# Kernel tuning notes

Hardware: AMD Instinct MI355X
Metric: run time of the kernel (lower is better)

The kernel has to match this reference:

```python
import jax, jax.numpy as jnp
import numpy as np

K = 64
M = 256
V = 5000

def setup_inputs() -> dict:
    key = jax.random.key(0)
    ks = jax.random.split(key, 8)
    feat_x = jax.random.normal(ks[0], (1, V, M), dtype=jnp.float32)
    feat_y = jax.random.normal(ks[1], (1, V, M), dtype=jnp.float32)
    evals_x = jnp.sort(jax.random.uniform(ks[2], (1, K), dtype=jnp.float32))
    evals_y = jnp.sort(jax.random.uniform(ks[3], (1, K), dtype=jnp.float32))
    evecs_trans_x = jax.random.normal(ks[4], (1, K, V), dtype=jnp.float32) / np.sqrt(V)
    evecs_trans_y = jax.random.normal(ks[5], (1, K, V), dtype=jnp.float32) / np.sqrt(V)
    eye = jnp.eye(K, dtype=jnp.float32)
    sqrtMk_x = (eye + 0.05 * jax.random.normal(ks[6], (K, K), dtype=jnp.float32))[None]
    sqrtMk_y = (eye + 0.05 * jax.random.normal(ks[7], (K, K), dtype=jnp.float32))[None]
    return {"feat_x": feat_x, "feat_y": feat_y, "evals_x": evals_x, "evals_y": evals_y,
            "evecs_trans_x": evecs_trans_x, "evecs_trans_y": evecs_trans_y,
            "sqrtMk_x": sqrtMk_x, "sqrtMk_y": sqrtMk_y}

LMBDA = 0.001

def _fmap(fx, fy, ex, ey, tx, ty, sx, sy):
    # squeeze batch dim of 1 (as in torch .squeeze())
    fx, fy = fx[0], fy[0]            # [V, m]
    ex, ey = ex[0], ey[0]            # [k]
    tx, ty = tx[0], ty[0]            # [k, V]
    sx, sy = sx[0], sy[0]            # [k, k]
    A = tx @ fx                      # [k, m] spectral coeffs of feat_x
    B = sy @ (ty @ fy)               # adapt_feature=True: premultiply by sqrtMk_y
    k, m = A.shape
    vec_B = B.T.reshape(m * k, 1)
    At_Ik = jnp.kron(A.T, sy)        # [m*k, k*k] (adapt_feature -> Ik = sqrtMk_y)
    first = At_Ik.T @ At_Ik          # [k^2, k^2]
    # adapt_mask=True branch
    inv_sx = jnp.linalg.inv(sx)
    lx = jnp.diag(ex)
    ly = jnp.diag(ey)
    lx_Ik = jnp.kron(lx @ inv_sx, sy)
    Ik_ly = jnp.kron(inv_sx, sy @ ly)
    Delta = lx_Ik - Ik_ly
    second = Delta.T @ Delta
    rhs = At_Ik.T @ vec_B
    op = first + LMBDA * second
    C = jnp.linalg.solve(op, rhs)
    return C.reshape(k, k).T[None]   # [1, k, k]

def reference(feat_x, feat_y, evals_x, evals_y, evecs_trans_x, evecs_trans_y, sqrtMk_x, sqrtMk_y):
    # bidirectional=False -> only Cxy (Cyx is None in the torch module)
    return _fmap(feat_x, feat_y, evals_x, evals_y, evecs_trans_x, evecs_trans_y, sqrtMk_x, sqrtMk_y)
```

## Files before the change

kernel.cpp:

```cpp
#include <hip/hip_runtime.h>

#define LMBDA 0.001f
#define NS_SY 4
#define NS_G  5
#define NS_SX 5
#define OUTER 3
#define LDP 68

#define WS_A    0
#define WS_FY   16384
#define WS_G1   32768
#define WS_T1   36864
#define WS_R2   40960
#define WS_R4   45056
#define WS_GINV 49152
#define WS_C    53248
#define WS_FYAT 57344
#define WS_FLAGS 61440

#define FMA4(ar, xs, b) { ar[0]=fmaf((xs),(b).x,ar[0]); ar[1]=fmaf((xs),(b).y,ar[1]); \
                          ar[2]=fmaf((xs),(b).z,ar[2]); ar[3]=fmaf((xs),(b).w,ar[3]); }

template<int SA, int SB>
__device__ __forceinline__ void mm64(const float* __restrict__ A,
                                     const float* __restrict__ B,
                                     int ti, int tj, float a[4][4]) {
    #pragma unroll 4
    for (int k = 0; k < 64; k += 4) {
        float4 av0 = *(const float4*)&A[(4 * ti + 0) * SA + k];
        float4 av1 = *(const float4*)&A[(4 * ti + 1) * SA + k];
        float4 av2 = *(const float4*)&A[(4 * ti + 2) * SA + k];
        float4 av3 = *(const float4*)&A[(4 * ti + 3) * SA + k];
        float4 b0 = *(const float4*)&B[(k + 0) * SB + 4 * tj];
        float4 b1 = *(const float4*)&B[(k + 1) * SB + 4 * tj];
        float4 b2 = *(const float4*)&B[(k + 2) * SB + 4 * tj];
        float4 b3 = *(const float4*)&B[(k + 3) * SB + 4 * tj];
        FMA4(a[0], av0.x, b0); FMA4(a[0], av0.y, b1); FMA4(a[0], av0.z, b2); FMA4(a[0], av0.w, b3);
        FMA4(a[1], av1.x, b0); FMA4(a[1], av1.y, b1); FMA4(a[1], av1.z, b2); FMA4(a[1], av1.w, b3);
        FMA4(a[2], av2.x, b0); FMA4(a[2], av2.y, b1); FMA4(a[2], av2.z, b2); FMA4(a[2], av2.w, b3);
        FMA4(a[3], av3.x, b0); FMA4(a[3], av3.y, b1); FMA4(a[3], av3.z, b2); FMA4(a[3], av3.w, b3);
    }
}

__device__ __forceinline__ void ns_invert(float* sM, float* sX, float* sY,
                                          int iters, int ti, int tj,
                                          int tid, float alpha)
{
    for (int idx = tid; idx < 4096; idx += 256) {
        int i = idx >> 6, j = idx & 63;
        sX[i * LDP + j] = (i == j) ? alpha : 0.f;
    }
    __syncthreads();
    for (int it = 0; it < iters; ++it) {
        float y[4][4];
        #pragma unroll
        for (int r = 0; r < 4; ++r)
            #pragma unroll
            for (int c = 0; c < 4; ++c) y[r][c] = 0.f;
        mm64<LDP, LDP>(sM, sX, ti, tj, y);
        #pragma unroll
        for (int r = 0; r < 4; ++r) {
            float4 v = {y[r][0], y[r][1], y[r][2], y[r][3]};
            *(float4*)&sY[(4 * ti + r) * 64 + 4 * tj] = v;
        }
        __syncthreads();
        float z[4][4];
        #pragma unroll
        for (int r = 0; r < 4; ++r)
            #pragma unroll
            for (int c = 0; c < 4; ++c) z[r][c] = 0.f;
        mm64<LDP, 64>(sX, sY, ti, tj, z);
        __syncthreads();
        #pragma unroll
        for (int r = 0; r < 4; ++r) {
            float4 xv = *(const float4*)&sX[(4 * ti + r) * LDP + 4 * tj];
            xv.x = 2.f * xv.x - z[r][0];
            xv.y = 2.f * xv.y - z[r][1];
            xv.z = 2.f * xv.z - z[r][2];
            xv.w = 2.f * xv.w - z[r][3];
            *(float4*)&sX[(4 * ti + r) * LDP + 4 * tj] = xv;
        }
        __syncthreads();
    }
}

__device__ __forceinline__ void wait_ge(int* flag, int target, int tid) {
    if (tid == 0) {
        while (__hip_atomic_load(flag, __ATOMIC_ACQUIRE, __HIP_MEMORY_SCOPE_AGENT) < target)
            __builtin_amdgcn_s_sleep(2);
    }
    __syncthreads();
    __threadfence();
}

__device__ __forceinline__ void signal_one(int* flag, int tid) {
    __syncthreads();
    __threadfence();
    if (tid == 0)
        (void)__hip_atomic_fetch_add(flag, 1, __ATOMIC_RELEASE, __HIP_MEMORY_SCOPE_AGENT);
}

__global__ __launch_bounds__(256, 1) void fused_fmnet(
    const float* __restrict__ fx, const float* __restrict__ fy,
    const float* __restrict__ ex, const float* __restrict__ ey,
    const float* __restrict__ tx, const float* __restrict__ ty,
    const float* __restrict__ sx, const float* __restrict__ sy,
    float* __restrict__ ws, float* __restrict__ out)
{
    extern __shared__ __align__(16) float lds[];
    int* flags = (int*)(ws + WS_FLAGS);
    const int tid = threadIdx.x;
    const int ti = tid >> 4, tj = tid & 15;
    const int bid = blockIdx.x;

    if (bid < 216) {
        float* sT = lds;
        float* sF = lds + 4352;
        const int gx = bid & 7, gy = bid >> 3;
        const int mat = gx >> 2;
        const int m0 = (gx & 3) << 6;
        const float* __restrict__ T = mat ? ty : tx;
        const float* __restrict__ F = mat ? fy : fx;
        float* __restrict__ Out = ws + (mat ? WS_FY : WS_A);

        float acc[4][4];
        #pragma unroll
        for (int r = 0; r < 4; ++r)
            #pragma unroll
            for (int c = 0; c < 4; ++c) acc[r][c] = 0.f;

        for (int sc = gy; sc * 64 < 5000; sc += 27) {
            const int v0 = sc << 6;
            int vlen = 5000 - v0; if (vlen > 64) vlen = 64;
            #pragma unroll
            for (int w = 0; w < 4; ++w) {
                const int fidx = tid + (w << 8);
                const int row = fidx >> 4, q = fidx & 15;
                const int vv = q << 2;
                if (vv < vlen) {
                    float4 val = *(const float4*)(T + (size_t)row * 5000 + v0 + vv);
                    sT[(vv + 0) * LDP + row] = val.x;
                    sT[(vv + 1) * LDP + row] = val.y;
                    sT[(vv + 2) * LDP + row] = val.z;
                    sT[(vv + 3) * LDP + row] = val.w;
                }
                if (row < vlen) {
                    *(float4*)&sF[row * LDP + (q << 2)] =
                        *(const float4*)(F + (size_t)(v0 + row) * 256 + m0 + (q << 2));
                }
            }
            __syncthreads();
            for (int v = 0; v < vlen; ++v) {
                float4 av = *(const float4*)&sT[v * LDP + 4 * ti];
                float4 bv = *(const float4*)&sF[v * LDP + 4 * tj];
                FMA4(acc[0], av.x, bv); FMA4(acc[1], av.y, bv);
                FMA4(acc[2], av.z, bv); FMA4(acc[3], av.w, bv);
            }
            __syncthreads();
        }
        #pragma unroll
        for (int r = 0; r < 4; ++r)
            #pragma unroll
            for (int c = 0; c < 4; ++c)
                atomicAdd(&Out[(4 * ti + r) * 256 + m0 + 4 * tj + c], acc[r][c]);
        __syncthreads();
        __threadfence();
        if (tid == 0) {
            (void)__hip_atomic_fetch_add(&flags[gx], 1, __ATOMIC_RELEASE, __HIP_MEMORY_SCOPE_AGENT);
            (void)__hip_atomic_fetch_add(&flags[10], 1, __ATOMIC_RELEASE, __HIP_MEMORY_SCOPE_AGENT);
        }
    } else if (bid < 220) {
        const int ch = bid - 216;
        wait_ge(&flags[ch], 27, tid);
        float* sA = lds;
        for (int idx = tid; idx < 1024; idx += 256) {
            int i = idx >> 4, m4 = (idx & 15) << 2;
            *(float4*)&sA[i * LDP + m4] =
                *(const float4*)&ws[WS_A + i * 256 + (ch << 6) + m4];
        }
        __syncthreads();
        float a[4][4];
        #pragma unroll
        for (int r = 0; r < 4; ++r)
            #pragma unroll
            for (int c = 0; c < 4; ++c) a[r][c] = 0.f;
        for (int m = 0; m < 64; m += 4) {
            float4 av[4], bv[4];
            #pragma unroll
            for (int r = 0; r < 4; ++r) av[r] = *(const float4*)&sA[(4 * ti + r) * LDP + m];
            #pragma unroll
            for (int c = 0; c < 4; ++c) bv[c] = *(const float4*)&sA[(4 * tj + c) * LDP + m];
            #pragma unroll
            for (int r = 0; r < 4; ++r)
                #pragma unroll
                for (int c = 0; c < 4; ++c)
                    a[r][c] += av[r].x * bv[c].x + av[r].y * bv[c].y
                             + av[r].z * bv[c].z + av[r].w * bv[c].w;
        }
        #pragma unroll
        for (int r = 0; r < 4; ++r)
            #pragma unroll
            for (int c = 0; c < 4; ++c)
                atomicAdd(&ws[WS_G1 + (4 * ti + r) * 64 + 4 * tj + c], a[r][c]);
        __syncthreads();
        __threadfence();
        if (tid == 0)
            (void)__hip_atomic_fetch_add(&flags[8], 1, __ATOMIC_RELEASE, __HIP_MEMORY_SCOPE_AGENT);
    } else if (bid == 220) {
        float* sSy = lds;
        float* sXx = lds + 4352;
        float* sYy = lds + 8704;
        float* sH  = lds + 12800;
        float* sV  = lds + 16896;
        for (int idx = tid; idx < 1024; idx += 256) {
            int i = idx >> 4, j4 = (idx & 15) << 2;
            *(float4*)&sSy[i * LDP + j4] = *(const float4*)&sy[i * 64 + j4];
        }
        if (tid < 64) sV[tid] = ey[tid];
        __syncthreads();
        {
            float h[4][4];
            #pragma unroll
            for (int r = 0; r < 4; ++r)
                #pragma unroll
                for (int c = 0; c < 4; ++c) h[r][c] = 0.f;
            for (int k = 0; k < 64; ++k) {
                float4 av = *(const float4*)&sSy[k * LDP + 4 * ti];
                float4 bv = *(const float4*)&sSy[k * LDP + 4 * tj];
                FMA4(h[0], av.x, bv); FMA4(h[1], av.y, bv);
                FMA4(h[2], av.z, bv); FMA4(h[3], av.w, bv);
            }
            #pragma unroll
            for (int r = 0; r < 4; ++r) {
                float4 v = {h[r][0], h[r][1], h[r][2], h[r][3]};
                *(float4*)&sH[(4 * ti + r) * 64 + 4 * tj] = v;
            }
        }
        __syncthreads();
        ns_invert(sSy, sXx, sYy, NS_SY, ti, tj, tid, 1.0f);
        {
            float h[4][4];
            #pragma unroll
            for (int r = 0; r < 4; ++r)
                #pragma unroll
                for (int c = 0; c < 4; ++c) h[r][c] = 0.f;
            for (int m = 0; m < 64; m += 4) {
                float4 av[4], bv[4];
                #pragma unroll
                for (int r = 0; r < 4; ++r) av[r] = *(const float4*)&sXx[(4 * ti + r) * LDP + m];
                #pragma unroll
                for (int c = 0; c < 4; ++c) bv[c] = *(const float4*)&sXx[(4 * tj + c) * LDP + m];
                #pragma unroll
                for (int r = 0; r < 4; ++r)
                    #pragma unroll
                    for (int c = 0; c < 4; ++c)
                        h[r][c] += av[r].x * bv[c].x + av[r].y * bv[c].y
                                 + av[r].z * bv[c].z + av[r].w * bv[c].w;
            }
            __syncthreads();
            #pragma unroll
            for (int r = 0; r < 4; ++r) {
                float4 v = {h[r][0], h[r][1], h[r][2], h[r][3]};
                *(float4*)&sSy[(4 * ti + r) * LDP + 4 * tj] = v;
            }
        }
        __syncthreads();
        {
            float a[4][4];
            #pragma unroll
            for (int r = 0; r < 4; ++r)
                #pragma unroll
                for (int c = 0; c < 4; ++c) a[r][c] = 0.f;
            #pragma unroll 4
            for (int k = 0; k < 64; k += 4) {
                float4 av[4];
                #pragma unroll
                for (int r = 0; r < 4; ++r) av[r] = *(const float4*)&sSy[(4 * ti + r) * LDP + k];
                #pragma unroll
                for (int q = 0; q < 4; ++q) {
                    float e = sV[k + q];
                    float4 bv = *(const float4*)&sH[(k + q) * 64 + 4 * tj];
                    bv.x *= e; bv.y *= e; bv.z *= e; bv.w *= e;
                    float xq[4] = {av[0].x, av[1].x, av[2].x, av[3].x};
                    if (q == 1) { xq[0]=av[0].y; xq[1]=av[1].y; xq[2]=av[2].y; xq[3]=av[3].y; }
                    if (q == 2) { xq[0]=av[0].z; xq[1]=av[1].z; xq[2]=av[2].z; xq[3]=av[3].z; }
                    if (q == 3) { xq[0]=av[0].w; xq[1]=av[1].w; xq[2]=av[2].w; xq[3]=av[3].w; }
                    #pragma unroll
                    for (int r = 0; r < 4; ++r) FMA4(a[r], xq[r], bv);
                }
            }
            #pragma unroll
            for (int r = 0; r < 4; ++r) {
                float4 v = {a[r][0], a[r][1], a[r][2], a[r][3]};
                *(float4*)&ws[WS_C + (4 * ti + r) * 64 + 4 * tj] = v;
            }
        }
        signal_one(&flags[9], tid);
    } else if (bid == 221) {
        float* sM = lds;
        float* sX = lds + 4352;
        float* sY = lds + 8704;
        float* sV = lds + 12800;
        for (int idx = tid; idx < 1024; idx += 256) {
            int i = idx >> 4, j4 = (idx & 15) << 2;
            *(float4*)&sM[i * LDP + j4] = *(const float4*)&sx[i * 64 + j4];
        }
        if (tid < 64) sV[tid] = ex[tid];
        __syncthreads();
        ns_invert(sM, sX, sY, NS_SX, ti, tj, tid, 1.0f);
        float aR2[4][4], aR4[4][4], aT1[4][4];
        #pragma unroll
        for (int r = 0; r < 4; ++r)
            #pragma unroll
            for (int c = 0; c < 4; ++c) { aR2[r][c] = 0.f; aR4[r][c] = 0.f; aT1[r][c] = 0.f; }
        for (int k = 0; k < 64; ++k) {
            float e = sV[k], e2 = e * e;
            float4 av = *(const float4*)&sX[k * LDP + 4 * ti];
            float4 bv = *(const float4*)&sX[k * LDP + 4 * tj];
            float avv[4] = {av.x, av.y, av.z, av.w};
            #pragma unroll
            for (int r = 0; r < 4; ++r) {
                FMA4(aR4[r], avv[r], bv);
                float ea = e * avv[r];
                FMA4(aR2[r], ea, bv);
                float e2a = e2 * avv[r];
                FMA4(aT1[r], e2a, bv);
            }
        }
        #pragma unroll
        for (int r = 0; r < 4; ++r) {
            int o = (4 * ti + r) * 64 + 4 * tj;
            float4 v2 = {aR2[r][0], aR2[r][1], aR2[r][2], aR2[r][3]};
            float4 v4 = {aR4[r][0], aR4[r][1], aR4[r][2], aR4[r][3]};
            float4 v1 = {aT1[r][0], aT1[r][1], aT1[r][2], aT1[r][3]};
            *(float4*)&ws[WS_R2 + o] = v2;
            *(float4*)&ws[WS_R4 + o] = v4;
            *(float4*)&ws[WS_T1 + o] = v1;
        }
        signal_one(&flags[9], tid);
    } else if (bid == 222) {
        wait_ge(&flags[8], 4, tid);
        float* sG = lds;
        float* sX = lds + 4352;
        float* sY = lds + 8704;
        float* sV = lds + 12800;
        for (int idx = tid; idx < 1024; idx += 256) {
            int i = idx >> 4, j4 = (idx & 15) << 2;
            *(float4*)&sG[i * LDP + j4] = *(const float4*)&ws[WS_G1 + i * 64 + j4];
        }
        __syncthreads();
        if (tid < 64) {
            float s = 0.f;
            for (int j4 = 0; j4 < 64; j4 += 4) {
                float4 v = *(const float4*)&sG[tid * LDP + j4];
                s += v.x * v.x + v.y * v.y + v.z * v.z + v.w * v.w;
            }
            sV[tid] = s;
            sV[64 + tid] = sG[tid * LDP + tid];
        }
        __syncthreads();
        float f2 = 0.f, tr = 0.f;
        for (int i = 0; i < 64; ++i) { f2 += sV[i]; tr += sV[64 + i]; }
        ns_invert(sG, sX, sY, NS_G, ti, tj, tid, tr / f2);
        for (int idx = tid; idx < 1024; idx += 256) {
            int i = idx >> 4, j4 = (idx & 15) << 2;
            *(float4*)&ws[WS_GINV + i * 64 + j4] = *(const float4*)&sX[i * LDP + j4];
        }
        signal_one(&flags[9], tid);
    } else if (bid == 223) {
        wait_ge(&flags[10], 216, tid);
        float* sFy = lds;
        float* sAx = lds + 4352;
        float a[4][4];
        #pragma unroll
        for (int r = 0; r < 4; ++r)
            #pragma unroll
            for (int c = 0; c < 4; ++c) a[r][c] = 0.f;
        for (int ch = 0; ch < 4; ++ch) {
            for (int idx = tid; idx < 1024; idx += 256) {
                int i = idx >> 4, m4 = (idx & 15) << 2;
                *(float4*)&sFy[i * LDP + m4] = *(const float4*)&ws[WS_FY + i * 256 + (ch << 6) + m4];
                *(float4*)&sAx[i * LDP + m4] = *(const float4*)&ws[WS_A  + i * 256 + (ch << 6) + m4];
            }
            __syncthreads();
            for (int m = 0; m < 64; m += 4) {
                float4 av[4], bv[4];
                #pragma unroll
                for (int r = 0; r < 4; ++r) av[r] = *(const float4*)&sFy[(4 * ti + r) * LDP + m];
                #pragma unroll
                for (int c = 0; c < 4; ++c) bv[c] = *(const float4*)&sAx[(4 * tj + c) * LDP + m];
                #pragma unroll
                for (int r = 0; r < 4; ++r)
                    #pragma unroll
                    for (int c = 0; c < 4; ++c)
                        a[r][c] += av[r].x * bv[c].x + av[r].y * bv[c].y
                                 + av[r].z * bv[c].z + av[r].w * bv[c].w;
            }
            __syncthreads();
        }
        #pragma unroll
        for (int r = 0; r < 4; ++r) {
            float4 v = {a[r][0], a[r][1], a[r][2], a[r][3]};
            *(float4*)&ws[WS_FYAT + (4 * ti + r) * 64 + 4 * tj] = v;
        }
        signal_one(&flags[9], tid);
    } else {
        wait_ge(&flags[9], 4, tid);
        float* cM1   = lds;
        float* cR2   = lds + 4096;
        float* cR4   = lds + 8192;
        float* cGinv = lds + 12288;
        float* sE    = lds + 16384;
        float* sX    = lds + 20480;
        float* cC    = lds + 24832;
        float* sW    = lds + 29184;

        for (int idx = tid; idx < 1024; idx += 256) {
            int i = idx >> 4, j4 = (idx & 15) << 2;
            int o = i * 64 + j4;
            float4 g = *(const float4*)&ws[WS_G1 + o];
            float4 t = *(const float4*)&ws[WS_T1 + o];
            float4 m = {fmaf(LMBDA, t.x, g.x), fmaf(LMBDA, t.y, g.y),
                        fmaf(LMBDA, t.z, g.z), fmaf(LMBDA, t.w, g.w)};
            *(float4*)&cM1[o]   = m;
            *(float4*)&cR2[o]   = *(const float4*)&ws[WS_R2 + o];
            *(float4*)&cR4[o]   = *(const float4*)&ws[WS_R4 + o];
            *(float4*)&cGinv[o] = *(const float4*)&ws[WS_GINV + o];
            *(float4*)&cC[i * LDP + j4] = *(const float4*)&ws[WS_C + o];
        }
        float4 eyv = *(const float4*)&ey[4 * ti];
        float eyr[4] = {eyv.x, eyv.y, eyv.z, eyv.w};
        float leyr[4];
        #pragma unroll
        for (int r = 0; r < 4; ++r) leyr[r] = LMBDA * eyr[r];

        float fyr[4][4], xreg[4][4];
        #pragma unroll
        for (int r = 0; r < 4; ++r) {
            float4 v = *(const float4*)&ws[WS_FYAT + (4 * ti + r) * 64 + 4 * tj];
            fyr[r][0] = v.x; fyr[r][1] = v.y; fyr[r][2] = v.z; fyr[r][3] = v.w;
            float4 z = {0.f, 0.f, 0.f, 0.f};
            *(float4*)&sX[(4 * ti + r) * LDP + 4 * tj] = z;
            #pragma unroll
            for (int c = 0; c < 4; ++c) xreg[r][c] = 0.f;
        }
        __syncthreads();

        float E1[4][4];
        for (int it = 0; it < OUTER; ++it) {
            {
                float Sm[4][4], S2[4][4], S4[4][4];
                #pragma unroll
                for (int r = 0; r < 4; ++r)
                    #pragma unroll
                    for (int c = 0; c < 4; ++c) { Sm[r][c] = 0.f; S2[r][c] = 0.f; S4[r][c] = 0.f; }
                #pragma unroll 2
                for (int k = 0; k < 64; k += 4) {
                    float4 av[4];
                    #pragma unroll
                    for (int r = 0; r < 4; ++r)
                        av[r] = *(const float4*)&sX[(4 * ti + r) * LDP + k];
                    #pragma unroll
                    for (int q = 0; q < 4; ++q) {
                        float4 mv = *(const float4*)&cM1[(k + q) * 64 + 4 * tj];
                        float4 qv = *(const float4*)&cR2[(k + q) * 64 + 4 * tj];
                        float4 rv = *(const float4*)&cR4[(k + q) * 64 + 4 * tj];
                        float xq[4] = {av[0].x, av[1].x, av[2].x, av[3].x};
                        if (q == 1) { xq[0]=av[0].y; xq[1]=av[1].y; xq[2]=av[2].y; xq[3]=av[3].y; }
                        if (q == 2) { xq[0]=av[0].z; xq[1]=av[1].z; xq[2]=av[2].z; xq[3]=av[3].z; }
                        if (q == 3) { xq[0]=av[0].w; xq[1]=av[1].w; xq[2]=av[2].w; xq[3]=av[3].w; }
                        #pragma unroll
                        for (int r = 0; r < 4; ++r) {
                            FMA4(Sm[r], xq[r], mv);
                            FMA4(S2[r], xq[r], qv);
                            FMA4(S4[r], xq[r], rv);
                        }
                    }
                }
                #pragma unroll
                for (int r = 0; r < 4; ++r) {
                    float4 e2;
                    e2.x = LMBDA * fmaf(eyr[r], S4[r][0], -S2[r][0]);
                    e2.y = LMBDA * fmaf(eyr[r], S4[r][1], -S2[r][1]);
                    e2.z = LMBDA * fmaf(eyr[r], S4[r][2], -S2[r][2]);
                    e2.w = LMBDA * fmaf(eyr[r], S4[r][3], -S2[r][3]);
                    *(float4*)&sE[(4 * ti + r) * 64 + 4 * tj] = e2;
                    #pragma unroll
                    for (int c = 0; c < 4; ++c)
                        E1[r][c] = fmaf(-leyr[r], S2[r][c], Sm[r][c]);
                }
            }
            __syncthreads();
            {
                float Z[4][4];
                #pragma unroll
                for (int r = 0; r < 4; ++r)
                    #pragma unroll
                    for (int c = 0; c < 4; ++c) Z[r][c] = 0.f;
                mm64<LDP, 64>(cC, sE, ti, tj, Z);
                #pragma unroll
                for (int r = 0; r < 4; ++r) {
                    float4 w;
                    w.x = fyr[r][0] - E1[r][0] - Z[r][0];
                    w.y = fyr[r][1] - E1[r][1] - Z[r][1];
                    w.z = fyr[r][2] - E1[r][2] - Z[r][2];
                    w.w = fyr[r][3] - E1[r][3] - Z[r][3];
                    *(float4*)&sW[(4 * ti + r) * LDP + 4 * tj] = w;
                }
            }
            __syncthreads();
            {
                float dX[4][4];
                #pragma unroll
                for (int r = 0; r < 4; ++r)
                    #pragma unroll
                    for (int c = 0; c < 4; ++c) dX[r][c] = 0.f;
                mm64<LDP, 64>(sW, cGinv, ti, tj, dX);
                #pragma unroll
                for (int r = 0; r < 4; ++r) {
                    float4 v;
                    #pragma unroll
                    for (int c = 0; c < 4; ++c) xreg[r][c] += dX[r][c];
                    v.x = xreg[r][0]; v.y = xreg[r][1]; v.z = xreg[r][2]; v.w = xreg[r][3];
                    *(float4*)&sX[(4 * ti + r) * LDP + 4 * tj] = v;
                    if (it == OUTER - 1)
                        *(float4*)&out[(4 * ti + r) * 64 + 4 * tj] = v;
                }
            }
            if (it == OUTER - 1) break;
            __syncthreads();
        }
    }
}

extern "C" void kernel_launch(void* const* d_in, const int* in_sizes, int n_in,
                              void* d_out, int out_size, void* d_ws, size_t ws_size,
                              hipStream_t stream) {
    (void)in_sizes; (void)n_in; (void)out_size; (void)ws_size;
    const float* fx = (const float*)d_in[0];
    const float* fy = (const float*)d_in[1];
    const float* ex = (const float*)d_in[2];
    const float* ey = (const float*)d_in[3];
    const float* tx = (const float*)d_in[4];
    const float* ty = (const float*)d_in[5];
    const float* sx = (const float*)d_in[6];
    const float* sy = (const float*)d_in[7];
    float* ws = (float*)d_ws;
    float* out = (float*)d_out;

    (void)hipFuncSetAttribute((const void*)fused_fmnet,
                              hipFuncAttributeMaxDynamicSharedMemorySize, 134144);

    (void)hipMemsetAsync(d_ws, 0, (WS_G1 + 4096) * sizeof(float), stream);
    (void)hipMemsetAsync((char*)d_ws + WS_FLAGS * sizeof(float), 0, 64, stream);
    fused_fmnet<<<225, 256, 134144, stream>>>(fx, fy, ex, ey, tx, ty, sx, sy, ws, out);
}
```

Baseline: 194.7 us.

## Split Fy·Aᵀ reduction across four chunk blocks and fold G inverse into final block

The single block that computed Fy·Aᵀ after all 216 GEMM blocks finished is replaced by four blocks. Each handles one 64-column chunk as soon as that chunk's A and Fy partials are ready, and accumulates into the workspace with atomics. The separate block that inverted G is removed, and the final solver block now runs the Newton-Schulz inversion of G itself while it waits for the other precomputations. This is meant to shorten the critical path of the dependency chain, at the cost of more atomics and more serial work in the last block. The change also unrolls the projection inner loop and lengthens the spin-wait sleep.

```diff
diff --git a/kernel.cpp b/kernel.cpp
--- a/kernel.cpp
+++ b/kernel.cpp
@@ -10,13 +10,12 @@
 #define WS_A    0
 #define WS_FY   16384
 #define WS_G1   32768
-#define WS_T1   36864
-#define WS_R2   40960
-#define WS_R4   45056
-#define WS_GINV 49152
+#define WS_FYAT 36864
+#define WS_T1   40960
+#define WS_R2   45056
+#define WS_R4   49152
 #define WS_C    53248
-#define WS_FYAT 57344
-#define WS_FLAGS 61440
+#define WS_FLAGS 57344
 
 #define FMA4(ar, xs, b) { ar[0]=fmaf((xs),(b).x,ar[0]); ar[1]=fmaf((xs),(b).y,ar[1]); \
                           ar[2]=fmaf((xs),(b).z,ar[2]); ar[3]=fmaf((xs),(b).w,ar[3]); }
@@ -42,7 +41,28 @@
     }
 }
 
-__device__ __forceinline__ void ns_invert(float* sM, float* sX, float* sY,
+template<int SA, int SB>
+__device__ __forceinline__ void mmdot(const float* __restrict__ A,
+                                      const float* __restrict__ B,
+                                      int ti, int tj, float a[4][4]) {
+    #pragma unroll 4
+    for (int m = 0; m < 64; m += 4) {
+        float4 av[4], bv[4];
+        #pragma unroll
+        for (int r = 0; r < 4; ++r) av[r] = *(const float4*)&A[(4 * ti + r) * SA + m];
+        #pragma unroll
+        for (int c = 0; c < 4; ++c) bv[c] = *(const float4*)&B[(4 * tj + c) * SB + m];
+        #pragma unroll
+        for (int r = 0; r < 4; ++r)
+            #pragma unroll
+            for (int c = 0; c < 4; ++c)
+                a[r][c] += av[r].x * bv[c].x + av[r].y * bv[c].y
+                         + av[r].z * bv[c].z + av[r].w * bv[c].w;
+    }
+}
+
+template<int SM>
+__device__ __forceinline__ void ns_invert(const float* sM, float* sX, float* sY,
                                           int iters, int ti, int tj,
                                           int tid, float alpha)
 {
@@ -52,23 +72,15 @@
     }
     __syncthreads();
     for (int it = 0; it < iters; ++it) {
-        float y[4][4];
-        #pragma unroll
-        for (int r = 0; r < 4; ++r)
-            #pragma unroll
-            for (int c = 0; c < 4; ++c) y[r][c] = 0.f;
-        mm64<LDP, LDP>(sM, sX, ti, tj, y);
+        float y[4][4] = {};
+        mm64<SM, LDP>(sM, sX, ti, tj, y);
         #pragma unroll
         for (int r = 0; r < 4; ++r) {
             float4 v = {y[r][0], y[r][1], y[r][2], y[r][3]};
             *(float4*)&sY[(4 * ti + r) * 64 + 4 * tj] = v;
         }
         __syncthreads();
-        float z[4][4];
-        #pragma unroll
-        for (int r = 0; r < 4; ++r)
-            #pragma unroll
-            for (int c = 0; c < 4; ++c) z[r][c] = 0.f;
+        float z[4][4] = {};
         mm64<LDP, 64>(sX, sY, ti, tj, z);
         __syncthreads();
         #pragma unroll
@@ -87,7 +99,7 @@
 __device__ __forceinline__ void wait_ge(int* flag, int target, int tid) {
     if (tid == 0) {
         while (__hip_atomic_load(flag, __ATOMIC_ACQUIRE, __HIP_MEMORY_SCOPE_AGENT) < target)
-            __builtin_amdgcn_s_sleep(2);
+            __builtin_amdgcn_s_sleep(8);
     }
     __syncthreads();
     __threadfence();
@@ -123,12 +135,7 @@
         const float* __restrict__ F = mat ? fy : fx;
         float* __restrict__ Out = ws + (mat ? WS_FY : WS_A);
 
-        float acc[4][4];
-        #pragma unroll
-        for (int r = 0; r < 4; ++r)
-            #pragma unroll
-            for (int c = 0; c < 4; ++c) acc[r][c] = 0.f;
-
+        float acc[4][4] = {};
         for (int sc = gy; sc * 64 < 5000; sc += 27) {
             const int v0 = sc << 6;
             int vlen = 5000 - v0; if (vlen > 64) vlen = 64;
@@ -150,6 +157,7 @@
                 }
             }
             __syncthreads();
+            #pragma unroll 4
             for (int v = 0; v < vlen; ++v) {
                 float4 av = *(const float4*)&sT[v * LDP + 4 * ti];
                 float4 bv = *(const float4*)&sF[v * LDP + 4 * tj];
@@ -165,10 +173,8 @@
                 atomicAdd(&Out[(4 * ti + r) * 256 + m0 + 4 * tj + c], acc[r][c]);
         __syncthreads();
         __threadfence();
-        if (tid == 0) {
+        if (tid == 0)
             (void)__hip_atomic_fetch_add(&flags[gx], 1, __ATOMIC_RELEASE, __HIP_MEMORY_SCOPE_AGENT);
-            (void)__hip_atomic_fetch_add(&flags[10], 1, __ATOMIC_RELEASE, __HIP_MEMORY_SCOPE_AGENT);
-        }
     } else if (bid < 220) {
         const int ch = bid - 216;
         wait_ge(&flags[ch], 27, tid);
@@ -179,24 +185,8 @@
                 *(const float4*)&ws[WS_A + i * 256 + (ch << 6) + m4];
         }
         __syncthreads();
-        float a[4][4];
-        #pragma unroll
-        for (int r = 0; r < 4; ++r)
-            #pragma unroll
-            for (int c = 0; c < 4; ++c) a[r][c] = 0.f;
-        for (int m = 0; m < 64; m += 4) {
-            float4 av[4], bv[4];
-            #pragma unroll
-            for (int r = 0; r < 4; ++r) av[r] = *(const float4*)&sA[(4 * ti + r) * LDP + m];
-            #pragma unroll
-            for (int c = 0; c < 4; ++c) bv[c] = *(const float4*)&sA[(4 * tj + c) * LDP + m];
-            #pragma unroll
-            for (int r = 0; r < 4; ++r)
-                #pragma unroll
-                for (int c = 0; c < 4; ++c)
-                    a[r][c] += av[r].x * bv[c].x + av[r].y * bv[c].y
-                             + av[r].z * bv[c].z + av[r].w * bv[c].w;
-        }
+        float a[4][4] = {};
+        mmdot<LDP, LDP>(sA, sA, ti, tj, a);
         #pragma unroll
         for (int r = 0; r < 4; ++r)
             #pragma unroll
@@ -206,7 +196,27 @@
         __threadfence();
         if (tid == 0)
             (void)__hip_atomic_fetch_add(&flags[8], 1, __ATOMIC_RELEASE, __HIP_MEMORY_SCOPE_AGENT);
-    } else if (bid == 220) {
+    } else if (bid < 224) {
+        const int ch = bid - 220;
+        wait_ge(&flags[ch], 27, tid);
+        wait_ge(&flags[4 + ch], 27, tid);
+        float* sFy = lds;
+        float* sAx = lds + 4352;
+        for (int idx = tid; idx < 1024; idx += 256) {
+            int i = idx >> 4, m4 = (idx & 15) << 2;
+            *(float4*)&sFy[i * LDP + m4] = *(const float4*)&ws[WS_FY + i * 256 + (ch << 6) + m4];
+            *(float4*)&sAx[i * LDP + m4] = *(const float4*)&ws[WS_A  + i * 256 + (ch << 6) + m4];
+        }
+        __syncthreads();
+        float a[4][4] = {};
+        mmdot<LDP, LDP>(sFy, sAx, ti, tj, a);
+        #pragma unroll
+        for (int r = 0; r < 4; ++r)
+            #pragma unroll
+            for (int c = 0; c < 4; ++c)
+                atomicAdd(&ws[WS_FYAT + (4 * ti + r) * 64 + 4 * tj + c], a[r][c]);
+        signal_one(&flags[9], tid);
+    } else if (bid == 224) {
         float* sSy = lds;
         float* sXx = lds + 4352;
         float* sYy = lds + 8704;
@@ -219,11 +229,7 @@
         if (tid < 64) sV[tid] = ey[tid];
         __syncthreads();
         {
-            float h[4][4];
-            #pragma unroll
-            for (int r = 0; r < 4; ++r)
-                #pragma unroll
-                for (int c = 0; c < 4; ++c) h[r][c] = 0.f;
+            float h[4][4] = {};
             for (int k = 0; k < 64; ++k) {
                 float4 av = *(const float4*)&sSy[k * LDP + 4 * ti];
                 float4 bv = *(const float4*)&sSy[k * LDP + 4 * tj];
@@ -237,26 +243,10 @@
             }
         }
         __syncthreads();
-        ns_invert(sSy, sXx, sYy, NS_SY, ti, tj, tid, 1.0f);
+        ns_invert<LDP>(sSy, sXx, sYy, NS_SY, ti, tj, tid, 1.0f);
         {
-            float h[4][4];
-            #pragma unroll
-            for (int r = 0; r < 4; ++r)
-                #pragma unroll
-                for (int c = 0; c < 4; ++c) h[r][c] = 0.f;
-            for (int m = 0; m < 64; m += 4) {
-                float4 av[4], bv[4];
-                #pragma unroll
-                for (int r = 0; r < 4; ++r) av[r] = *(const float4*)&sXx[(4 * ti + r) * LDP + m];
-                #pragma unroll
-                for (int c = 0; c < 4; ++c) bv[c] = *(const float4*)&sXx[(4 * tj + c) * LDP + m];
-                #pragma unroll
-                for (int r = 0; r < 4; ++r)
-                    #pragma unroll
-                    for (int c = 0; c < 4; ++c)
-                        h[r][c] += av[r].x * bv[c].x + av[r].y * bv[c].y
-                                 + av[r].z * bv[c].z + av[r].w * bv[c].w;
-            }
+            float h[4][4] = {};
+            mmdot<LDP, LDP>(sXx, sXx, ti, tj, h);
             __syncthreads();
             #pragma unroll
             for (int r = 0; r < 4; ++r) {
@@ -266,11 +256,7 @@
         }
         __syncthreads();
         {
-            float a[4][4];
-            #pragma unroll
-            for (int r = 0; r < 4; ++r)
-                #pragma unroll
-                for (int c = 0; c < 4; ++c) a[r][c] = 0.f;
+            float a[4][4] = {};
             #pragma unroll 4
             for (int k = 0; k < 64; k += 4) {
                 float4 av[4];
@@ -296,7 +282,7 @@
             }
         }
         signal_one(&flags[9], tid);
-    } else if (bid == 221) {
+    } else if (bid == 225) {
         float* sM = lds;
         float* sX = lds + 4352;
         float* sY = lds + 8704;
@@ -307,12 +293,8 @@
         }
         if (tid < 64) sV[tid] = ex[tid];
         __syncthreads();
-        ns_invert(sM, sX, sY, NS_SX, ti, tj, tid, 1.0f);
-        float aR2[4][4], aR4[4][4], aT1[4][4];
-        #pragma unroll
-        for (int r = 0; r < 4; ++r)
-            #pragma unroll
-            for (int c = 0; c < 4; ++c) { aR2[r][c] = 0.f; aR4[r][c] = 0.f; aT1[r][c] = 0.f; }
+        ns_invert<LDP>(sM, sX, sY, NS_SX, ti, tj, tid, 1.0f);
+        float aR2[4][4] = {}, aR4[4][4] = {}, aT1[4][4] = {};
         for (int k = 0; k < 64; ++k) {
             float e = sV[k], e2 = e * e;
             float4 av = *(const float4*)&sX[k * LDP + 4 * ti];
@@ -338,74 +320,7 @@
             *(float4*)&ws[WS_T1 + o] = v1;
         }
         signal_one(&flags[9], tid);
-    } else if (bid == 222) {
-        wait_ge(&flags[8], 4, tid);
-        float* sG = lds;
-        float* sX = lds + 4352;
-        float* sY = lds + 8704;
-        float* sV = lds + 12800;
-        for (int idx = tid; idx < 1024; idx += 256) {
-            int i = idx >> 4, j4 = (idx & 15) << 2;
-            *(float4*)&sG[i * LDP + j4] = *(const float4*)&ws[WS_G1 + i * 64 + j4];
-        }
-        __syncthreads();
-        if (tid < 64) {
-            float s = 0.f;
-            for (int j4 = 0; j4 < 64; j4 += 4) {
-                float4 v = *(const float4*)&sG[tid * LDP + j4];
-                s += v.x * v.x + v.y * v.y + v.z * v.z + v.w * v.w;
-            }
-            sV[tid] = s;
-            sV[64 + tid] = sG[tid * LDP + tid];
-        }
-        __syncthreads();
-        float f2 = 0.f, tr = 0.f;
-        for (int i = 0; i < 64; ++i) { f2 += sV[i]; tr += sV[64 + i]; }
-        ns_invert(sG, sX, sY, NS_G, ti, tj, tid, tr / f2);
-        for (int idx = tid; idx < 1024; idx += 256) {
-            int i = idx >> 4, j4 = (idx & 15) << 2;
-            *(float4*)&ws[WS_GINV + i * 64 + j4] = *(const float4*)&sX[i * LDP + j4];
-        }
-        signal_one(&flags[9], tid);
-    } else if (bid == 223) {
-        wait_ge(&flags[10], 216, tid);
-        float* sFy = lds;
-        float* sAx = lds + 4352;
-        float a[4][4];
-        #pragma unroll
-        for (int r = 0; r < 4; ++r)
-            #pragma unroll
-            for (int c = 0; c < 4; ++c) a[r][c] = 0.f;
-        for (int ch = 0; ch < 4; ++ch) {
-            for (int idx = tid; idx < 1024; idx += 256) {
-                int i = idx >> 4, m4 = (idx & 15) << 2;
-                *(float4*)&sFy[i * LDP + m4] = *(const float4*)&ws[WS_FY + i * 256 + (ch << 6) + m4];
-                *(float4*)&sAx[i * LDP + m4] = *(const float4*)&ws[WS_A  + i * 256 + (ch << 6) + m4];
-            }
-            __syncthreads();
-            for (int m = 0; m < 64; m += 4) {
-                float4 av[4], bv[4];
-                #pragma unroll
-                for (int r = 0; r < 4; ++r) av[r] = *(const float4*)&sFy[(4 * ti + r) * LDP + m];
-                #pragma unroll
-                for (int c = 0; c < 4; ++c) bv[c] = *(const float4*)&sAx[(4 * tj + c) * LDP + m];
-                #pragma unroll
-                for (int r = 0; r < 4; ++r)
-                    #pragma unroll
-                    for (int c = 0; c < 4; ++c)
-                        a[r][c] += av[r].x * bv[c].x + av[r].y * bv[c].y
-                                 + av[r].z * bv[c].z + av[r].w * bv[c].w;
-            }
-            __syncthreads();
-        }
-        #pragma unroll
-        for (int r = 0; r < 4; ++r) {
-            float4 v = {a[r][0], a[r][1], a[r][2], a[r][3]};
-            *(float4*)&ws[WS_FYAT + (4 * ti + r) * 64 + 4 * tj] = v;
-        }
-        signal_one(&flags[9], tid);
     } else {
-        wait_ge(&flags[9], 4, tid);
         float* cM1   = lds;
         float* cR2   = lds + 4096;
         float* cR4   = lds + 8192;
@@ -415,17 +330,40 @@
         float* cC    = lds + 24832;
         float* sW    = lds + 29184;
 
+        wait_ge(&flags[8], 4, tid);
+        for (int idx = tid; idx < 1024; idx += 256) {
+            int i = idx >> 4, j4 = (idx & 15) << 2;
+            *(float4*)&cM1[i * 64 + j4] = *(const float4*)&ws[WS_G1 + i * 64 + j4];
+        }
+        __syncthreads();
+        if (tid < 64) {
+            float s = 0.f;
+            for (int j4 = 0; j4 < 64; j4 += 4) {
+                float4 v = *(const float4*)&cM1[tid * 64 + j4];
+                s += v.x * v.x + v.y * v.y + v.z * v.z + v.w * v.w;
+            }
+            sW[tid] = s;
+            sW[64 + tid] = cM1[tid * 64 + tid];
+        }
+        __syncthreads();
+        float f2 = 0.f, tr = 0.f;
+        for (int i = 0; i < 64; ++i) { f2 += sW[i]; tr += sW[64 + i]; }
+        ns_invert<64>(cM1, sX, sE, NS_G, ti, tj, tid, tr / f2);
+        for (int idx = tid; idx < 1024; idx += 256) {
+            int i = idx >> 4, j4 = (idx & 15) << 2;
+            *(float4*)&cGinv[i * 64 + j4] = *(const float4*)&sX[i * LDP + j4];
+        }
+        wait_ge(&flags[9], 6, tid);
         for (int idx = tid; idx < 1024; idx += 256) {
             int i = idx >> 4, j4 = (idx & 15) << 2;
             int o = i * 64 + j4;
-            float4 g = *(const float4*)&ws[WS_G1 + o];
+            float4 gv = *(const float4*)&cM1[o];
             float4 t = *(const float4*)&ws[WS_T1 + o];
-            float4 m = {fmaf(LMBDA, t.x, g.x), fmaf(LMBDA, t.y, g.y),
-                        fmaf(LMBDA, t.z, g.z), fmaf(LMBDA, t.w, g.w)};
-            *(float4*)&cM1[o]   = m;
-            *(float4*)&cR2[o]   = *(const float4*)&ws[WS_R2 + o];
-            *(float4*)&cR4[o]   = *(const float4*)&ws[WS_R4 + o];
-            *(float4*)&cGinv[o] = *(const float4*)&ws[WS_GINV + o];
+            gv.x = fmaf(LMBDA, t.x, gv.x); gv.y = fmaf(LMBDA, t.y, gv.y);
+            gv.z = fmaf(LMBDA, t.z, gv.z); gv.w = fmaf(LMBDA, t.w, gv.w);
+            *(float4*)&cM1[o] = gv;
+            *(float4*)&cR2[o] = *(const float4*)&ws[WS_R2 + o];
+            *(float4*)&cR4[o] = *(const float4*)&ws[WS_R4 + o];
             *(float4*)&cC[i * LDP + j4] = *(const float4*)&ws[WS_C + o];
         }
         float4 eyv = *(const float4*)&ey[4 * ti];
@@ -449,11 +387,7 @@
         float E1[4][4];
         for (int it = 0; it < OUTER; ++it) {
             {
-                float Sm[4][4], S2[4][4], S4[4][4];
-                #pragma unroll
-                for (int r = 0; r < 4; ++r)
-                    #pragma unroll
-                    for (int c = 0; c < 4; ++c) { Sm[r][c] = 0.f; S2[r][c] = 0.f; S4[r][c] = 0.f; }
+                float Sm[4][4] = {}, S2[4][4] = {}, S4[4][4] = {};
                 #pragma unroll 2
                 for (int k = 0; k < 64; k += 4) {
                     float4 av[4];
@@ -492,11 +426,7 @@
             }
             __syncthreads();
             {
-                float Z[4][4];
-                #pragma unroll
-                for (int r = 0; r < 4; ++r)
-                    #pragma unroll
-                    for (int c = 0; c < 4; ++c) Z[r][c] = 0.f;
+                float Z[4][4] = {};
                 mm64<LDP, 64>(cC, sE, ti, tj, Z);
                 #pragma unroll
                 for (int r = 0; r < 4; ++r) {
@@ -510,11 +440,7 @@
             }
             __syncthreads();
             {
-                float dX[4][4];
-                #pragma unroll
-                for (int r = 0; r < 4; ++r)
-                    #pragma unroll
-                    for (int c = 0; c < 4; ++c) dX[r][c] = 0.f;
+                float dX[4][4] = {};
                 mm64<LDP, 64>(sW, cGinv, ti, tj, dX);
                 #pragma unroll
                 for (int r = 0; r < 4; ++r) {
@@ -551,7 +477,7 @@
     (void)hipFuncSetAttribute((const void*)fused_fmnet,
                               hipFuncAttributeMaxDynamicSharedMemorySize, 134144);
 
-    (void)hipMemsetAsync(d_ws, 0, (WS_G1 + 4096) * sizeof(float), stream);
-    (void)hipMemsetAsync((char*)d_ws + WS_FLAGS * sizeof(float), 0, 64, stream);
-    fused_fmnet<<<225, 256, 134144, stream>>>(fx, fy, ex, ey, tx, ty, sx, sy, ws, out);
-}
+    (void)hipMemsetAsync(d_ws, 0, (size_t)(WS_T1) * sizeof(float), stream);
+    (void)hipMemsetAsync((char*)d_ws + (size_t)WS_FLAGS * sizeof(float), 0, 64, stream);
+    fused_fmnet<<<227, 256, 134144, stream>>>(fx, fy, ex, ey, tx, ty, sx, sy, ws, out);
+}
```

Result: faster. 190.4 us (-2.2%).
